# Optimization experiments

Measured on AMD Instinct MI355X. Metric: run time of the kernel, lower is better.

The kernel has to match this reference:

```python
import jax, jax.numpy as jnp
import numpy as np

B, T, I, H, O = 64, 512, 256, 512, 256

def setup_inputs() -> dict:
    key = jax.random.key(0)
    ks = jax.random.split(key, 12)
    s = 1.0 / np.sqrt(H)
    u = lambda k, shp: jax.random.uniform(k, shp, jnp.float32, -s, s)
    return {
        'x': jax.random.normal(ks[0], (B, T, I), jnp.float32),
        'w_ih0': u(ks[1], (H, I)),  'w_hh0': u(ks[2], (H, H)),
        'b_ih0': u(ks[3], (H,)),    'b_hh0': u(ks[4], (H,)),
        'w_ih1': u(ks[5], (H, H)),  'w_hh1': u(ks[6], (H, H)),
        'b_ih1': u(ks[7], (H,)),    'b_hh1': u(ks[8], (H,)),
        'fc_w': u(ks[9], (O, H)),   'fc_b': u(ks[10], (O,)),
    }

def _rnn_layer(inp, w_ih, w_hh, b_ih, b_hh):
    # inp: [B, T, F] -> precompute input projection once (one big GEMM)
    xp = jnp.einsum('btf,hf->bth', inp, w_ih) + b_ih + b_hh  # [B, T, H]
    def step(h, xt):
        h = jnp.tanh(xt + h @ w_hh.T)  # [B, H]
        return h, h
    h0 = jnp.zeros((inp.shape[0], w_hh.shape[0]), inp.dtype)
    hT, outs = jax.lax.scan(step, h0, jnp.swapaxes(xp, 0, 1))  # outs: [T, B, H]
    return jnp.swapaxes(outs, 0, 1), hT

def reference(x, w_ih0, w_hh0, b_ih0, b_hh0, w_ih1, w_hh1, b_ih1, b_hh1, fc_w, fc_b):
    out0, h0f = _rnn_layer(x, w_ih0, w_hh0, b_ih0, b_hh0)
    out1, h1f = _rnn_layer(out0, w_ih1, w_hh1, b_ih1, b_hh1)
    hidden = jnp.stack([h0f, h1f])                  # [n_layers, B, H]
    out = out1.reshape(-1, out1.shape[-1]) @ fc_w.T + fc_b  # [B*T, O]
    return out, hidden
```

## Files before the change

kernel.cpp:

```cpp
#include <hip/hip_runtime.h>

#define B_  64
#define T_  512
#define I_  256
#define H_  512
#define O_  256
#define JW  2
#define BS  16
#define NG  (B_ / BS)
#define SENT 0x7F7F7F7Fu
#define SLOT_BYTES 8192
#define BLK_SLOT_STRIDE 32768

typedef __attribute__((ext_vector_type(8))) __bf16 bf16x8;
typedef __attribute__((ext_vector_type(4))) float f32x4;
typedef unsigned int u32x4 __attribute__((ext_vector_type(4)));

__device__ __forceinline__ unsigned short f2bf(float f) {
    unsigned int u = __float_as_uint(f);
    unsigned int r = (u + 0x7fffu + ((u >> 16) & 1u)) >> 16;
    return (unsigned short)r;
}

__device__ __forceinline__ float tanh_fast(float x) {
    float e = __expf(2.0f * x);
    float d = e + 1.0f;
    float r;
    asm("v_rcp_f32 %0, %1" : "=v"(r) : "v"(d));
    return 1.0f - 2.0f * r;
}

__global__ void cvt_kernel(const float* __restrict__ in, unsigned short* __restrict__ out, int n4) {
    int i = blockIdx.x * blockDim.x + threadIdx.x;
    if (i >= n4) return;
    float4 f = reinterpret_cast<const float4*>(in)[i];
    ushort4 o;
    o.x = f2bf(f.x); o.y = f2bf(f.y); o.z = f2bf(f.z); o.w = f2bf(f.w);
    reinterpret_cast<ushort4*>(out)[i] = o;
}

__global__ __launch_bounds__(256) void gemm_kernel(
    const unsigned short* __restrict__ A,
    const unsigned short* __restrict__ Bw,
    const float* __restrict__ b0,
    const float* __restrict__ b1,
    float* __restrict__ C,
    int M, int N, int K)
{
    const int m0 = blockIdx.x * 64;
    const int n0 = blockIdx.y * 64;
    const int tid = threadIdx.x;
    const int wv = tid >> 6;
    const int l = tid & 63;
    const int lr = l & 15;
    const int lk = (l >> 4) * 8;
    const int arow = m0 + wv * 16 + lr;

    f32x4 acc[4] = {{0,0,0,0},{0,0,0,0},{0,0,0,0},{0,0,0,0}};
    const int nks = K / 32;
    for (int ks = 0; ks < nks; ++ks) {
        bf16x8 a = *reinterpret_cast<const bf16x8*>(A + (size_t)arow * K + ks * 32 + lk);
        #pragma unroll
        for (int nt = 0; nt < 4; ++nt) {
            bf16x8 b = *reinterpret_cast<const bf16x8*>(Bw + (size_t)(n0 + nt * 16 + lr) * K + ks * 32 + lk);
            acc[nt] = __builtin_amdgcn_mfma_f32_16x16x32_bf16(a, b, acc[nt], 0, 0, 0);
        }
    }
    #pragma unroll
    for (int nt = 0; nt < 4; ++nt) {
        #pragma unroll
        for (int r = 0; r < 4; ++r) {
            int row = m0 + wv * 16 + (l >> 4) * 4 + r;
            int col = n0 + nt * 16 + lr;
            float v = acc[nt][r];
            if (b0) v += b0[col];
            if (b1) v += b1[col];
            C[(size_t)row * N + col] = v;
        }
    }
}

#define LDW8(ARR, BASE) \
    asm volatile( \
        "global_load_dwordx4 %0, %8, %9 offset:0\n\t" \
        "global_load_dwordx4 %1, %8, %9 offset:64\n\t" \
        "global_load_dwordx4 %2, %8, %9 offset:128\n\t" \
        "global_load_dwordx4 %3, %8, %9 offset:192\n\t" \
        "global_load_dwordx4 %4, %8, %9 offset:256\n\t" \
        "global_load_dwordx4 %5, %8, %9 offset:320\n\t" \
        "global_load_dwordx4 %6, %8, %9 offset:384\n\t" \
        "global_load_dwordx4 %7, %8, %9 offset:448\n\t" \
        "s_waitcnt vmcnt(0)" \
        : "=&v"(ARR[0]), "=&v"(ARR[1]), "=&v"(ARR[2]), "=&v"(ARR[3]), \
          "=&v"(ARR[4]), "=&v"(ARR[5]), "=&v"(ARR[6]), "=&v"(ARR[7]) \
        : "v"(BASE), "s"(w))

#define STORE_SLOT_OUT(PK, VSLW, VOUT) \
    asm volatile( \
        "global_store_dword %16, %0, %21 sc0 sc1\n\t" \
        "global_store_dword %16, %1, %21 offset:512 sc0 sc1\n\t" \
        "global_store_dword %16, %2, %21 offset:1024 sc0 sc1\n\t" \
        "global_store_dword %16, %3, %21 offset:1536 sc0 sc1\n\t" \
        "global_store_dword %16, %4, %21 offset:32 sc0 sc1\n\t" \
        "global_store_dword %16, %5, %21 offset:544 sc0 sc1\n\t" \
        "global_store_dword %16, %6, %21 offset:1056 sc0 sc1\n\t" \
        "global_store_dword %16, %7, %21 offset:1568 sc0 sc1\n\t" \
        "global_store_dword %16, %8, %21 offset:64 sc0 sc1\n\t" \
        "global_store_dword %16, %9, %21 offset:576 sc0 sc1\n\t" \
        "global_store_dword %16, %10, %21 offset:1088 sc0 sc1\n\t" \
        "global_store_dword %16, %11, %21 offset:1600 sc0 sc1\n\t" \
        "global_store_dword %16, %12, %21 offset:96 sc0 sc1\n\t" \
        "global_store_dword %16, %13, %21 offset:608 sc0 sc1\n\t" \
        "global_store_dword %16, %14, %21 offset:1120 sc0 sc1\n\t" \
        "global_store_dword %16, %15, %21 offset:1632 sc0 sc1\n\t" \
        "global_store_dword %17, %0, %22\n\t" \
        "global_store_dword %18, %1, %22\n\t" \
        "global_store_dword %19, %2, %22\n\t" \
        "global_store_dword %20, %3, %22\n\t" \
        "global_store_dword %17, %4, %22 offset:32\n\t" \
        "global_store_dword %18, %5, %22 offset:32\n\t" \
        "global_store_dword %19, %6, %22 offset:32\n\t" \
        "global_store_dword %20, %7, %22 offset:32\n\t" \
        "global_store_dword %17, %8, %22 offset:64\n\t" \
        "global_store_dword %18, %9, %22 offset:64\n\t" \
        "global_store_dword %19, %10, %22 offset:64\n\t" \
        "global_store_dword %20, %11, %22 offset:64\n\t" \
        "global_store_dword %17, %12, %22 offset:96\n\t" \
        "global_store_dword %18, %13, %22 offset:96\n\t" \
        "global_store_dword %19, %14, %22 offset:96\n\t" \
        "global_store_dword %20, %15, %22 offset:96" \
        :: "v"(PK[0]), "v"(PK[1]), "v"(PK[2]), "v"(PK[3]), \
           "v"(PK[4]), "v"(PK[5]), "v"(PK[6]), "v"(PK[7]), \
           "v"(PK[8]), "v"(PK[9]), "v"(PK[10]), "v"(PK[11]), \
           "v"(PK[12]), "v"(PK[13]), "v"(PK[14]), "v"(PK[15]), \
           "v"(VSLW), "v"(VOUT[0]), "v"(VOUT[1]), "v"(VOUT[2]), "v"(VOUT[3]), \
           "s"(slots), "s"(out_bf) \
        : "memory")

__global__ __launch_bounds__(256, 1) void recur_kernel(
    const float* __restrict__ xp,
    const unsigned short* __restrict__ w,
    unsigned short* __restrict__ out_bf,
    float* __restrict__ h_final,
    unsigned short* __restrict__ slots)
{
    __shared__ __align__(16) unsigned short lds[16 * 280];

    const int bid = blockIdx.x;
    const int g   = bid >> 1;
    const int jw  = bid & 1;
    const int pjw = jw ^ 1;
    const int b0  = g * BS;
    const int tid = threadIdx.x;
    const int wv  = tid >> 6;
    const int l   = tid & 63;
    const int lr  = l & 15;
    const int lk  = (l >> 4) * 8;
    const int jn0 = jw * 256 + wv * 64;
    const int erow_l = (l >> 4) * 4;
    const int erow_g = b0 + erow_l;

    bf16x8 bwo[4][8], bwp[4][8];
    #pragma unroll
    for (int nt = 0; nt < 4; ++nt) {
        unsigned int vo = (unsigned)((jn0 + nt * 16 + lr) * (H_ * 2) + jw  * 512 + lk * 2);
        unsigned int vp = (unsigned)((jn0 + nt * 16 + lr) * (H_ * 2) + pjw * 512 + lk * 2);
        LDW8(bwo[nt], vo);
        LDW8(bwp[nt], vp);
    }

    unsigned int vxpr[4], vout[4];
    #pragma unroll
    for (int r = 0; r < 4; ++r) {
        vxpr[r] = (unsigned)((((erow_g + r) * T_) * H_ + jn0 + lr) * 4);
        vout[r] = (unsigned)(((erow_g + r) * T_) * H_ * 2 + (jn0 + lr) * 2);
    }
    const unsigned int slot_wr_b = (unsigned)(bid * BLK_SLOT_STRIDE);
    const unsigned int slot_rd_b = (unsigned)((bid ^ 1) * BLK_SLOT_STRIDE);
    const unsigned int vslr_base = slot_rd_b + (unsigned)(lr * 512 + lk * 2);
    const unsigned int vslw_base = slot_wr_b + (unsigned)(erow_l * 512 + (wv * 64 + lr) * 2);
    const unsigned int vsent_base = slot_rd_b + (unsigned)(wv * 2048 + l * 16);
    const u32x4 sentq = {SENT, SENT, SENT, SENT};

    {
        float xpr[16];
        asm volatile(
            "global_load_dword %0, %16, %20\n\t"
            "global_load_dword %1, %17, %20\n\t"
            "global_load_dword %2, %18, %20\n\t"
            "global_load_dword %3, %19, %20\n\t"
            "global_load_dword %4, %16, %20 offset:64\n\t"
            "global_load_dword %5, %17, %20 offset:64\n\t"
            "global_load_dword %6, %18, %20 offset:64\n\t"
            "global_load_dword %7, %19, %20 offset:64\n\t"
            "global_load_dword %8, %16, %20 offset:128\n\t"
            "global_load_dword %9, %17, %20 offset:128\n\t"
            "global_load_dword %10, %18, %20 offset:128\n\t"
            "global_load_dword %11, %19, %20 offset:128\n\t"
            "global_load_dword %12, %16, %20 offset:192\n\t"
            "global_load_dword %13, %17, %20 offset:192\n\t"
            "global_load_dword %14, %18, %20 offset:192\n\t"
            "global_load_dword %15, %19, %20 offset:192\n\t"
            "s_waitcnt vmcnt(0)"
            : "=&v"(xpr[0]), "=&v"(xpr[1]), "=&v"(xpr[2]), "=&v"(xpr[3]),
              "=&v"(xpr[4]), "=&v"(xpr[5]), "=&v"(xpr[6]), "=&v"(xpr[7]),
              "=&v"(xpr[8]), "=&v"(xpr[9]), "=&v"(xpr[10]), "=&v"(xpr[11]),
              "=&v"(xpr[12]), "=&v"(xpr[13]), "=&v"(xpr[14]), "=&v"(xpr[15])
            : "v"(vxpr[0]), "v"(vxpr[1]), "v"(vxpr[2]), "v"(vxpr[3]), "s"(xp));

        unsigned int pk[16];
        #pragma unroll
        for (int nt = 0; nt < 4; ++nt)
            #pragma unroll
            for (int r = 0; r < 4; ++r) {
                int i = nt * 4 + r;
                float hv = tanh_fast(xpr[i]);
                unsigned int mine = f2bf(hv);
                unsigned int oth = (unsigned int)__shfl_xor((int)mine, 1, 64);
                pk[i] = mine | (oth << 16);
            }
        if (!(lr & 1)) {
            unsigned int* lw = (unsigned int*)lds;
            const int cb = wv * 32 + (lr >> 1);
            #pragma unroll
            for (int nt = 0; nt < 4; ++nt)
                #pragma unroll
                for (int r = 0; r < 4; ++r)
                    lw[(erow_l + r) * 140 + cb + nt * 8] = pk[nt * 4 + r];
            unsigned int vslw = vslw_base + 1u * SLOT_BYTES;
            STORE_SLOT_OUT(pk, vslw, vout);
        }
        __syncthreads();
        #pragma unroll
        for (int r = 0; r < 4; ++r) { vxpr[r] += H_ * 4; vout[r] += H_ * 2; }
    }

    for (int t = 1; t < T_; ++t) {
        f32x4 acc[4] = {{0,0,0,0},{0,0,0,0},{0,0,0,0},{0,0,0,0}};
        {
            bf16x8 afo[8];
            const unsigned short* lrb = lds + lr * 280 + lk;
            #pragma unroll
            for (int i = 0; i < 8; ++i)
                afo[i] = *reinterpret_cast<const bf16x8*>(lrb + i * 32);
            #pragma unroll
            for (int i = 0; i < 8; ++i) {
                acc[0] = __builtin_amdgcn_mfma_f32_16x16x32_bf16(afo[i], bwo[0][i], acc[0], 0, 0, 0);
                acc[1] = __builtin_amdgcn_mfma_f32_16x16x32_bf16(afo[i], bwo[1][i], acc[1], 0, 0, 0);
                acc[2] = __builtin_amdgcn_mfma_f32_16x16x32_bf16(afo[i], bwo[2][i], acc[2], 0, 0, 0);
                acc[3] = __builtin_amdgcn_mfma_f32_16x16x32_bf16(afo[i], bwo[3][i], acc[3], 0, 0, 0);
            }
        }
        __builtin_amdgcn_sched_barrier(0);

        const unsigned int vslr = vslr_base + (unsigned)(t & 3) * SLOT_BYTES;
        float xpr[16];
        u32x4 afp[8];
        asm volatile(
            "global_load_dword %0, %24, %28\n\t"
            "global_load_dword %1, %25, %28\n\t"
            "global_load_dword %2, %26, %28\n\t"
            "global_load_dword %3, %27, %28\n\t"
            "global_load_dword %4, %24, %28 offset:64\n\t"
            "global_load_dword %5, %25, %28 offset:64\n\t"
            "global_load_dword %6, %26, %28 offset:64\n\t"
            "global_load_dword %7, %27, %28 offset:64\n\t"
            "global_load_dword %8, %24, %28 offset:128\n\t"
            "global_load_dword %9, %25, %28 offset:128\n\t"
            "global_load_dword %10, %26, %28 offset:128\n\t"
            "global_load_dword %11, %27, %28 offset:128\n\t"
            "global_load_dword %12, %24, %28 offset:192\n\t"
            "global_load_dword %13, %25, %28 offset:192\n\t"
            "global_load_dword %14, %26, %28 offset:192\n\t"
            "global_load_dword %15, %27, %28 offset:192\n\t"
            "global_load_dwordx4 %16, %29, %30 sc0 sc1\n\t"
            "global_load_dwordx4 %17, %29, %30 offset:64 sc0 sc1\n\t"
            "global_load_dwordx4 %18, %29, %30 offset:128 sc0 sc1\n\t"
            "global_load_dwordx4 %19, %29, %30 offset:192 sc0 sc1\n\t"
            "global_load_dwordx4 %20, %29, %30 offset:256 sc0 sc1\n\t"
            "global_load_dwordx4 %21, %29, %30 offset:320 sc0 sc1\n\t"
            "global_load_dwordx4 %22, %29, %30 offset:384 sc0 sc1\n\t"
            "global_load_dwordx4 %23, %29, %30 offset:448 sc0 sc1\n\t"
            "s_waitcnt vmcnt(0)"
            : "=&v"(xpr[0]), "=&v"(xpr[1]), "=&v"(xpr[2]), "=&v"(xpr[3]),
              "=&v"(xpr[4]), "=&v"(xpr[5]), "=&v"(xpr[6]), "=&v"(xpr[7]),
              "=&v"(xpr[8]), "=&v"(xpr[9]), "=&v"(xpr[10]), "=&v"(xpr[11]),
              "=&v"(xpr[12]), "=&v"(xpr[13]), "=&v"(xpr[14]), "=&v"(xpr[15]),
              "=&v"(afp[0]), "=&v"(afp[1]), "=&v"(afp[2]), "=&v"(afp[3]),
              "=&v"(afp[4]), "=&v"(afp[5]), "=&v"(afp[6]), "=&v"(afp[7])
            : "v"(vxpr[0]), "v"(vxpr[1]), "v"(vxpr[2]), "v"(vxpr[3]),
              "s"(xp), "v"(vslr), "s"(slots));

        int bad = 0;
        #pragma unroll
        for (int i = 0; i < 8; ++i)
            #pragma unroll
            for (int j = 0; j < 4; ++j)
                bad |= (afp[i][j] == SENT);
        while (__any(bad)) {
            asm volatile(
                "global_load_dwordx4 %0, %8, %9 sc0 sc1\n\t"
                "global_load_dwordx4 %1, %8, %9 offset:64 sc0 sc1\n\t"
                "global_load_dwordx4 %2, %8, %9 offset:128 sc0 sc1\n\t"
                "global_load_dwordx4 %3, %8, %9 offset:192 sc0 sc1\n\t"
                "global_load_dwordx4 %4, %8, %9 offset:256 sc0 sc1\n\t"
                "global_load_dwordx4 %5, %8, %9 offset:320 sc0 sc1\n\t"
                "global_load_dwordx4 %6, %8, %9 offset:384 sc0 sc1\n\t"
                "global_load_dwordx4 %7, %8, %9 offset:448 sc0 sc1\n\t"
                "s_waitcnt vmcnt(0)"
                : "=&v"(afp[0]), "=&v"(afp[1]), "=&v"(afp[2]), "=&v"(afp[3]),
                  "=&v"(afp[4]), "=&v"(afp[5]), "=&v"(afp[6]), "=&v"(afp[7])
                : "v"(vslr), "s"(slots));
            bad = 0;
            #pragma unroll
            for (int i = 0; i < 8; ++i)
                #pragma unroll
                for (int j = 0; j < 4; ++j)
                    bad |= (afp[i][j] == SENT);
        }
        __builtin_amdgcn_sched_barrier(0);

        #pragma unroll
        for (int i = 0; i < 8; ++i) {
            bf16x8 a = __builtin_bit_cast(bf16x8, afp[i]);
            acc[0] = __builtin_amdgcn_mfma_f32_16x16x32_bf16(a, bwp[0][i], acc[0], 0, 0, 0);
            acc[1] = __builtin_amdgcn_mfma_f32_16x16x32_bf16(a, bwp[1][i], acc[1], 0, 0, 0);
            acc[2] = __builtin_amdgcn_mfma_f32_16x16x32_bf16(a, bwp[2][i], acc[2], 0, 0, 0);
            acc[3] = __builtin_amdgcn_mfma_f32_16x16x32_bf16(a, bwp[3][i], acc[3], 0, 0, 0);
        }

        unsigned int pk[16];
        #pragma unroll
        for (int nt = 0; nt < 4; ++nt)
            #pragma unroll
            for (int r = 0; r < 4; ++r) {
                int i = nt * 4 + r;
                float pre = acc[nt][r] + xpr[i];
                float hv = tanh_fast(pre);
                if (t == T_ - 1)
                    h_final[(size_t)(erow_g + r) * H_ + jn0 + nt * 16 + lr] = hv;
                unsigned int mine = f2bf(hv);
                unsigned int oth = (unsigned int)__shfl_xor((int)mine, 1, 64);
                pk[i] = mine | (oth << 16);
            }
        if (!(lr & 1)) {
            unsigned int* lw = (unsigned int*)lds;
            const int cb = wv * 32 + (lr >> 1);
            #pragma unroll
            for (int nt = 0; nt < 4; ++nt)
                #pragma unroll
                for (int r = 0; r < 4; ++r)
                    lw[(erow_l + r) * 140 + cb + nt * 8] = pk[nt * 4 + r];
            unsigned int vslw = vslw_base + (unsigned)((t + 1) & 3) * SLOT_BYTES;
            STORE_SLOT_OUT(pk, vslw, vout);
        }

        __syncthreads();

        {
            unsigned int vs = vsent_base + (unsigned)(t & 3) * SLOT_BYTES;
            asm volatile(
                "global_store_dwordx4 %0, %1, %2 sc0 sc1\n\t"
                "global_store_dwordx4 %0, %1, %2 offset:1024 sc0 sc1"
                :: "v"(vs), "v"(sentq), "s"(slots) : "memory");
        }
        #pragma unroll
        for (int r = 0; r < 4; ++r) { vxpr[r] += H_ * 4; vout[r] += H_ * 2; }
    }
}

#define OFF_XBF    ((size_t)0)
#define OFF_WIH0   ((size_t)16777216)
#define OFF_WHH0   ((size_t)17039360)
#define OFF_WIH1   ((size_t)17563648)
#define OFF_WHH1   ((size_t)18087936)
#define OFF_FCW    ((size_t)18612224)
#define OFF_XP     ((size_t)18874368)
#define OFF_OUTBF  ((size_t)85983232)
#define OFF_SLOTS  ((size_t)119537664)
#define WS_NEED    ((size_t)119799808)

extern "C" void kernel_launch(void* const* d_in, const int* in_sizes, int n_in,
                              void* d_out, int out_size, void* d_ws, size_t ws_size,
                              hipStream_t stream) {
    if (ws_size < WS_NEED) return;
    const float* x     = (const float*)d_in[0];
    const float* w_ih0 = (const float*)d_in[1];
    const float* w_hh0 = (const float*)d_in[2];
    const float* b_ih0 = (const float*)d_in[3];
    const float* b_hh0 = (const float*)d_in[4];
    const float* w_ih1 = (const float*)d_in[5];
    const float* w_hh1 = (const float*)d_in[6];
    const float* b_ih1 = (const float*)d_in[7];
    const float* b_hh1 = (const float*)d_in[8];
    const float* fc_w  = (const float*)d_in[9];
    const float* fc_b  = (const float*)d_in[10];

    char* ws = (char*)d_ws;
    unsigned short* x_bf     = (unsigned short*)(ws + OFF_XBF);
    unsigned short* w_ih0_bf = (unsigned short*)(ws + OFF_WIH0);
    unsigned short* w_hh0_bf = (unsigned short*)(ws + OFF_WHH0);
    unsigned short* w_ih1_bf = (unsigned short*)(ws + OFF_WIH1);
    unsigned short* w_hh1_bf = (unsigned short*)(ws + OFF_WHH1);
    unsigned short* fc_w_bf  = (unsigned short*)(ws + OFF_FCW);
    float*          xp       = (float*)(ws + OFF_XP);
    unsigned short* out_bf   = (unsigned short*)(ws + OFF_OUTBF);
    unsigned short* slots    = (unsigned short*)(ws + OFF_SLOTS);

    float* out  = (float*)d_out;
    float* hid0 = out + (size_t)B_ * T_ * O_;
    float* hid1 = hid0 + (size_t)B_ * H_;

    hipMemsetAsync(ws + OFF_SLOTS, 0x7F, 262144, stream);

    auto cvt = [&](const float* in, unsigned short* o, int n) {
        int n4 = n / 4;
        cvt_kernel<<<(n4 + 255) / 256, 256, 0, stream>>>(in, o, n4);
    };
    cvt(x,     x_bf,     B_ * T_ * I_);
    cvt(w_ih0, w_ih0_bf, H_ * I_);
    cvt(w_hh0, w_hh0_bf, H_ * H_);
    cvt(w_ih1, w_ih1_bf, H_ * H_);
    cvt(w_hh1, w_hh1_bf, H_ * H_);
    cvt(fc_w,  fc_w_bf,  O_ * H_);

    const int M = B_ * T_;

    gemm_kernel<<<dim3(M / 64, H_ / 64), 256, 0, stream>>>(
        x_bf, w_ih0_bf, b_ih0, b_hh0, xp, M, H_, I_);

    recur_kernel<<<NG * JW, 256, 0, stream>>>(xp, w_hh0_bf, out_bf, hid0, slots);

    gemm_kernel<<<dim3(M / 64, H_ / 64), 256, 0, stream>>>(
        out_bf, w_ih1_bf, b_ih1, b_hh1, xp, M, H_, H_);

    hipMemsetAsync(ws + OFF_SLOTS, 0x7F, 262144, stream);

    recur_kernel<<<NG * JW, 256, 0, stream>>>(xp, w_hh1_bf, out_bf, hid1, slots);

    gemm_kernel<<<dim3(M / 64, O_ / 64), 256, 0, stream>>>(
        out_bf, fc_w_bf, fc_b, nullptr, out, M, O_, H_);
}
```

Measured before the change: 3.599 ms.

## Process two batch groups per block and permute xp layout for vector loads

The recurrence kernel now runs on 4 blocks instead of 8. Each block pair covers 32 batch rows split into two 16-row groups, so the MFMA work per exchanged step doubles and the number of cross-block handshakes per batch row halves. The input-projection GEMM writes its output in a permuted column order, which lets each lane fetch its 16 xp values with four dwordx4 loads instead of sixteen scalar loads. In exchange, each block does twice the serial work per timestep, and the two groups' peer loads and spin-waits are serialized within the step.

```diff
diff --git a/kernel.cpp b/kernel.cpp
--- a/kernel.cpp
+++ b/kernel.cpp
@@ -5,12 +5,9 @@
 #define I_  256
 #define H_  512
 #define O_  256
-#define JW  2
-#define BS  16
-#define NG  (B_ / BS)
 #define SENT 0x7F7F7F7Fu
-#define SLOT_BYTES 8192
-#define BLK_SLOT_STRIDE 32768
+#define SLOT_BYTES 16384
+#define BLK_SLOT_ELEMS 32768
 
 typedef __attribute__((ext_vector_type(8))) __bf16 bf16x8;
 typedef __attribute__((ext_vector_type(4))) float f32x4;
@@ -45,7 +42,7 @@
     const float* __restrict__ b0,
     const float* __restrict__ b1,
     float* __restrict__ C,
-    int M, int N, int K)
+    int M, int N, int K, int perm)
 {
     const int m0 = blockIdx.x * 64;
     const int n0 = blockIdx.y * 64;
@@ -75,7 +72,8 @@
             float v = acc[nt][r];
             if (b0) v += b0[col];
             if (b1) v += b1[col];
-            C[(size_t)row * N + col] = v;
+            int cs = perm ? ((col & 15) * 32 + (col >> 4)) : col;
+            C[(size_t)row * N + cs] = v;
         }
     }
 }
@@ -95,7 +93,51 @@
           "=&v"(ARR[4]), "=&v"(ARR[5]), "=&v"(ARR[6]), "=&v"(ARR[7]) \
         : "v"(BASE), "s"(w))
 
-#define STORE_SLOT_OUT(PK, VSLW, VOUT) \
+#define LOAD_XP_PEER(XPQ, AFP, VSLR, XPBASE, SLBASE) \
+    asm volatile( \
+        "global_load_dwordx4 %0, %12, %16\n\t" \
+        "global_load_dwordx4 %1, %13, %16\n\t" \
+        "global_load_dwordx4 %2, %14, %16\n\t" \
+        "global_load_dwordx4 %3, %15, %16\n\t" \
+        "global_load_dwordx4 %4, %17, %18 sc0 sc1\n\t" \
+        "global_load_dwordx4 %5, %17, %18 offset:64 sc0 sc1\n\t" \
+        "global_load_dwordx4 %6, %17, %18 offset:128 sc0 sc1\n\t" \
+        "global_load_dwordx4 %7, %17, %18 offset:192 sc0 sc1\n\t" \
+        "global_load_dwordx4 %8, %17, %18 offset:256 sc0 sc1\n\t" \
+        "global_load_dwordx4 %9, %17, %18 offset:320 sc0 sc1\n\t" \
+        "global_load_dwordx4 %10, %17, %18 offset:384 sc0 sc1\n\t" \
+        "global_load_dwordx4 %11, %17, %18 offset:448 sc0 sc1\n\t" \
+        "s_waitcnt vmcnt(0)" \
+        : "=&v"(XPQ[0]), "=&v"(XPQ[1]), "=&v"(XPQ[2]), "=&v"(XPQ[3]), \
+          "=&v"(AFP[0]), "=&v"(AFP[1]), "=&v"(AFP[2]), "=&v"(AFP[3]), \
+          "=&v"(AFP[4]), "=&v"(AFP[5]), "=&v"(AFP[6]), "=&v"(AFP[7]) \
+        : "v"(vxpr[0]), "v"(vxpr[1]), "v"(vxpr[2]), "v"(vxpr[3]), \
+          "s"(XPBASE), "v"(VSLR), "s"(SLBASE))
+
+#define RETRY8(AFP, VSLR, SLBASE) \
+    asm volatile( \
+        "global_load_dwordx4 %0, %8, %9 sc0 sc1\n\t" \
+        "global_load_dwordx4 %1, %8, %9 offset:64 sc0 sc1\n\t" \
+        "global_load_dwordx4 %2, %8, %9 offset:128 sc0 sc1\n\t" \
+        "global_load_dwordx4 %3, %8, %9 offset:192 sc0 sc1\n\t" \
+        "global_load_dwordx4 %4, %8, %9 offset:256 sc0 sc1\n\t" \
+        "global_load_dwordx4 %5, %8, %9 offset:320 sc0 sc1\n\t" \
+        "global_load_dwordx4 %6, %8, %9 offset:384 sc0 sc1\n\t" \
+        "global_load_dwordx4 %7, %8, %9 offset:448 sc0 sc1\n\t" \
+        "s_waitcnt vmcnt(0)" \
+        : "=&v"(AFP[0]), "=&v"(AFP[1]), "=&v"(AFP[2]), "=&v"(AFP[3]), \
+          "=&v"(AFP[4]), "=&v"(AFP[5]), "=&v"(AFP[6]), "=&v"(AFP[7]) \
+        : "v"(VSLR), "s"(SLBASE))
+
+#define SENT_CHECK(AFP, BAD) \
+    { BAD = 0; \
+      _Pragma("unroll") \
+      for (int _i = 0; _i < 8; ++_i) \
+          _Pragma("unroll") \
+          for (int _j = 0; _j < 4; ++_j) \
+              BAD |= (AFP[_i][_j] == SENT); }
+
+#define STORE_SLOT_OUT(PK, VSLW, SLWB, OUTB) \
     asm volatile( \
         "global_store_dword %16, %0, %21 sc0 sc1\n\t" \
         "global_store_dword %16, %1, %21 offset:512 sc0 sc1\n\t" \
@@ -133,8 +175,8 @@
            "v"(PK[4]), "v"(PK[5]), "v"(PK[6]), "v"(PK[7]), \
            "v"(PK[8]), "v"(PK[9]), "v"(PK[10]), "v"(PK[11]), \
            "v"(PK[12]), "v"(PK[13]), "v"(PK[14]), "v"(PK[15]), \
-           "v"(VSLW), "v"(VOUT[0]), "v"(VOUT[1]), "v"(VOUT[2]), "v"(VOUT[3]), \
-           "s"(slots), "s"(out_bf) \
+           "v"(VSLW), "v"(vout[0]), "v"(vout[1]), "v"(vout[2]), "v"(vout[3]), \
+           "s"(SLWB), "s"(OUTB) \
         : "memory")
 
 __global__ __launch_bounds__(256, 1) void recur_kernel(
@@ -144,13 +186,14 @@
     float* __restrict__ h_final,
     unsigned short* __restrict__ slots)
 {
-    __shared__ __align__(16) unsigned short lds[16 * 280];
+    __shared__ __align__(16) unsigned short lds[32 * 280];
 
     const int bid = blockIdx.x;
-    const int g   = bid >> 1;
+    const int g01 = bid >> 1;
     const int jw  = bid & 1;
     const int pjw = jw ^ 1;
-    const int b0  = g * BS;
+    const int b0A = g01 * 32;
+    const int b0B = g01 * 32 + 16;
     const int tid = threadIdx.x;
     const int wv  = tid >> 6;
     const int l   = tid & 63;
@@ -158,7 +201,16 @@
     const int lk  = (l >> 4) * 8;
     const int jn0 = jw * 256 + wv * 64;
     const int erow_l = (l >> 4) * 4;
-    const int erow_g = b0 + erow_l;
+
+    const float*          xpA  = xp     + (size_t)b0A * T_ * H_;
+    const float*          xpB  = xp     + (size_t)b0B * T_ * H_;
+    unsigned short*       outA = out_bf + (size_t)b0A * T_ * H_;
+    unsigned short*       outB = out_bf + (size_t)b0B * T_ * H_;
+    float*                hfA  = h_final + (size_t)b0A * H_;
+    float*                hfB  = h_final + (size_t)b0B * H_;
+    unsigned short*       slW  = slots + (size_t)bid * BLK_SLOT_ELEMS;
+    const unsigned short* slRA = slots + (size_t)(bid ^ 1) * BLK_SLOT_ELEMS;
+    const unsigned short* slRB = slRA + 4096;
 
     bf16x8 bwo[4][8], bwp[4][8];
     #pragma unroll
@@ -172,197 +224,158 @@
     unsigned int vxpr[4], vout[4];
     #pragma unroll
     for (int r = 0; r < 4; ++r) {
-        vxpr[r] = (unsigned)((((erow_g + r) * T_) * H_ + jn0 + lr) * 4);
-        vout[r] = (unsigned)(((erow_g + r) * T_) * H_ * 2 + (jn0 + lr) * 2);
-    }
-    const unsigned int slot_wr_b = (unsigned)(bid * BLK_SLOT_STRIDE);
-    const unsigned int slot_rd_b = (unsigned)((bid ^ 1) * BLK_SLOT_STRIDE);
-    const unsigned int vslr_base = slot_rd_b + (unsigned)(lr * 512 + lk * 2);
-    const unsigned int vslw_base = slot_wr_b + (unsigned)(erow_l * 512 + (wv * 64 + lr) * 2);
-    const unsigned int vsent_base = slot_rd_b + (unsigned)(wv * 2048 + l * 16);
+        vxpr[r] = (unsigned)(((erow_l + r) * T_ * H_ + lr * 32 + jw * 16 + wv * 4) * 4);
+        vout[r] = (unsigned)(((erow_l + r) * T_) * H_ * 2 + (jn0 + lr) * 2);
+    }
+    const unsigned int vslr0 = (unsigned)(lr * 512 + lk * 2);
+    const unsigned int vslw0 = (unsigned)(erow_l * 512 + (wv * 64 + lr) * 2);
+    const unsigned int vsent0 = (unsigned)(tid * 64);
     const u32x4 sentq = {SENT, SENT, SENT, SENT};
-
-    {
-        float xpr[16];
+    const int cb = wv * 32 + (lr >> 1);
+
+    #pragma unroll
+    for (int grp = 0; grp < 2; ++grp) {
+        const float* xpg = grp ? xpB : xpA;
+        unsigned short* outg = grp ? outB : outA;
+        f32x4 xpq[4];
         asm volatile(
-            "global_load_dword %0, %16, %20\n\t"
-            "global_load_dword %1, %17, %20\n\t"
-            "global_load_dword %2, %18, %20\n\t"
-            "global_load_dword %3, %19, %20\n\t"
-            "global_load_dword %4, %16, %20 offset:64\n\t"
-            "global_load_dword %5, %17, %20 offset:64\n\t"
-            "global_load_dword %6, %18, %20 offset:64\n\t"
-            "global_load_dword %7, %19, %20 offset:64\n\t"
-            "global_load_dword %8, %16, %20 offset:128\n\t"
-            "global_load_dword %9, %17, %20 offset:128\n\t"
-            "global_load_dword %10, %18, %20 offset:128\n\t"
-            "global_load_dword %11, %19, %20 offset:128\n\t"
-            "global_load_dword %12, %16, %20 offset:192\n\t"
-            "global_load_dword %13, %17, %20 offset:192\n\t"
-            "global_load_dword %14, %18, %20 offset:192\n\t"
-            "global_load_dword %15, %19, %20 offset:192\n\t"
+            "global_load_dwordx4 %0, %4, %8\n\t"
+            "global_load_dwordx4 %1, %5, %8\n\t"
+            "global_load_dwordx4 %2, %6, %8\n\t"
+            "global_load_dwordx4 %3, %7, %8\n\t"
             "s_waitcnt vmcnt(0)"
-            : "=&v"(xpr[0]), "=&v"(xpr[1]), "=&v"(xpr[2]), "=&v"(xpr[3]),
-              "=&v"(xpr[4]), "=&v"(xpr[5]), "=&v"(xpr[6]), "=&v"(xpr[7]),
-              "=&v"(xpr[8]), "=&v"(xpr[9]), "=&v"(xpr[10]), "=&v"(xpr[11]),
-              "=&v"(xpr[12]), "=&v"(xpr[13]), "=&v"(xpr[14]), "=&v"(xpr[15])
-            : "v"(vxpr[0]), "v"(vxpr[1]), "v"(vxpr[2]), "v"(vxpr[3]), "s"(xp));
-
+            : "=&v"(xpq[0]), "=&v"(xpq[1]), "=&v"(xpq[2]), "=&v"(xpq[3])
+            : "v"(vxpr[0]), "v"(vxpr[1]), "v"(vxpr[2]), "v"(vxpr[3]), "s"(xpg));
         unsigned int pk[16];
         #pragma unroll
         for (int nt = 0; nt < 4; ++nt)
             #pragma unroll
             for (int r = 0; r < 4; ++r) {
-                int i = nt * 4 + r;
-                float hv = tanh_fast(xpr[i]);
+                float hv = tanh_fast(xpq[r][nt]);
                 unsigned int mine = f2bf(hv);
                 unsigned int oth = (unsigned int)__shfl_xor((int)mine, 1, 64);
-                pk[i] = mine | (oth << 16);
+                pk[nt * 4 + r] = mine | (oth << 16);
             }
         if (!(lr & 1)) {
             unsigned int* lw = (unsigned int*)lds;
-            const int cb = wv * 32 + (lr >> 1);
             #pragma unroll
             for (int nt = 0; nt < 4; ++nt)
                 #pragma unroll
                 for (int r = 0; r < 4; ++r)
-                    lw[(erow_l + r) * 140 + cb + nt * 8] = pk[nt * 4 + r];
-            unsigned int vslw = vslw_base + 1u * SLOT_BYTES;
-            STORE_SLOT_OUT(pk, vslw, vout);
-        }
-        __syncthreads();
-        #pragma unroll
-        for (int r = 0; r < 4; ++r) { vxpr[r] += H_ * 4; vout[r] += H_ * 2; }
-    }
+                    lw[(grp * 16 + erow_l + r) * 140 + cb + nt * 8] = pk[nt * 4 + r];
+            unsigned int vslw = vslw0 + 1u * SLOT_BYTES + (unsigned)(grp * 8192);
+            STORE_SLOT_OUT(pk, vslw, slW, outg);
+        }
+    }
+    __syncthreads();
+    #pragma unroll
+    for (int r = 0; r < 4; ++r) { vxpr[r] += H_ * 4; vout[r] += H_ * 2; }
 
     for (int t = 1; t < T_; ++t) {
-        f32x4 acc[4] = {{0,0,0,0},{0,0,0,0},{0,0,0,0},{0,0,0,0}};
+        f32x4 accA[4] = {{0,0,0,0},{0,0,0,0},{0,0,0,0},{0,0,0,0}};
+        f32x4 accB[4] = {{0,0,0,0},{0,0,0,0},{0,0,0,0},{0,0,0,0}};
         {
             bf16x8 afo[8];
             const unsigned short* lrb = lds + lr * 280 + lk;
             #pragma unroll
-            for (int i = 0; i < 8; ++i)
-                afo[i] = *reinterpret_cast<const bf16x8*>(lrb + i * 32);
+            for (int i = 0; i < 8; ++i) afo[i] = *reinterpret_cast<const bf16x8*>(lrb + i * 32);
             #pragma unroll
             for (int i = 0; i < 8; ++i) {
-                acc[0] = __builtin_amdgcn_mfma_f32_16x16x32_bf16(afo[i], bwo[0][i], acc[0], 0, 0, 0);
-                acc[1] = __builtin_amdgcn_mfma_f32_16x16x32_bf16(afo[i], bwo[1][i], acc[1], 0, 0, 0);
-                acc[2] = __builtin_amdgcn_mfma_f32_16x16x32_bf16(afo[i], bwo[2][i], acc[2], 0, 0, 0);
-                acc[3] = __builtin_amdgcn_mfma_f32_16x16x32_bf16(afo[i], bwo[3][i], acc[3], 0, 0, 0);
+                accA[0] = __builtin_amdgcn_mfma_f32_16x16x32_bf16(afo[i], bwo[0][i], accA[0], 0, 0, 0);
+                accA[1] = __builtin_amdgcn_mfma_f32_16x16x32_bf16(afo[i], bwo[1][i], accA[1], 0, 0, 0);
+                accA[2] = __builtin_amdgcn_mfma_f32_16x16x32_bf16(afo[i], bwo[2][i], accA[2], 0, 0, 0);
+                accA[3] = __builtin_amdgcn_mfma_f32_16x16x32_bf16(afo[i], bwo[3][i], accA[3], 0, 0, 0);
             }
         }
+        {
+            bf16x8 afo[8];
+            const unsigned short* lrb = lds + (16 + lr) * 280 + lk;
+            #pragma unroll
+            for (int i = 0; i < 8; ++i) afo[i] = *reinterpret_cast<const bf16x8*>(lrb + i * 32);
+            #pragma unroll
+            for (int i = 0; i < 8; ++i) {
+                accB[0] = __builtin_amdgcn_mfma_f32_16x16x32_bf16(afo[i], bwo[0][i], accB[0], 0, 0, 0);
+                accB[1] = __builtin_amdgcn_mfma_f32_16x16x32_bf16(afo[i], bwo[1][i], accB[1], 0, 0, 0);
+                accB[2] = __builtin_amdgcn_mfma_f32_16x16x32_bf16(afo[i], bwo[2][i], accB[2], 0, 0, 0);
+                accB[3] = __builtin_amdgcn_mfma_f32_16x16x32_bf16(afo[i], bwo[3][i], accB[3], 0, 0, 0);
+            }
+        }
         __builtin_amdgcn_sched_barrier(0);
 
-        const unsigned int vslr = vslr_base + (unsigned)(t & 3) * SLOT_BYTES;
-        float xpr[16];
-        u32x4 afp[8];
-        asm volatile(
-            "global_load_dword %0, %24, %28\n\t"
-            "global_load_dword %1, %25, %28\n\t"
-            "global_load_dword %2, %26, %28\n\t"
-            "global_load_dword %3, %27, %28\n\t"
-            "global_load_dword %4, %24, %28 offset:64\n\t"
-            "global_load_dword %5, %25, %28 offset:64\n\t"
-            "global_load_dword %6, %26, %28 offset:64\n\t"
-            "global_load_dword %7, %27, %28 offset:64\n\t"
-            "global_load_dword %8, %24, %28 offset:128\n\t"
-            "global_load_dword %9, %25, %28 offset:128\n\t"
-            "global_load_dword %10, %26, %28 offset:128\n\t"
-            "global_load_dword %11, %27, %28 offset:128\n\t"
-            "global_load_dword %12, %24, %28 offset:192\n\t"
-            "global_load_dword %13, %25, %28 offset:192\n\t"
-            "global_load_dword %14, %26, %28 offset:192\n\t"
-            "global_load_dword %15, %27, %28 offset:192\n\t"
-            "global_load_dwordx4 %16, %29, %30 sc0 sc1\n\t"
-            "global_load_dwordx4 %17, %29, %30 offset:64 sc0 sc1\n\t"
-            "global_load_dwordx4 %18, %29, %30 offset:128 sc0 sc1\n\t"
-            "global_load_dwordx4 %19, %29, %30 offset:192 sc0 sc1\n\t"
-            "global_load_dwordx4 %20, %29, %30 offset:256 sc0 sc1\n\t"
-            "global_load_dwordx4 %21, %29, %30 offset:320 sc0 sc1\n\t"
-            "global_load_dwordx4 %22, %29, %30 offset:384 sc0 sc1\n\t"
-            "global_load_dwordx4 %23, %29, %30 offset:448 sc0 sc1\n\t"
-            "s_waitcnt vmcnt(0)"
-            : "=&v"(xpr[0]), "=&v"(xpr[1]), "=&v"(xpr[2]), "=&v"(xpr[3]),
-              "=&v"(xpr[4]), "=&v"(xpr[5]), "=&v"(xpr[6]), "=&v"(xpr[7]),
-              "=&v"(xpr[8]), "=&v"(xpr[9]), "=&v"(xpr[10]), "=&v"(xpr[11]),
-              "=&v"(xpr[12]), "=&v"(xpr[13]), "=&v"(xpr[14]), "=&v"(xpr[15]),
-              "=&v"(afp[0]), "=&v"(afp[1]), "=&v"(afp[2]), "=&v"(afp[3]),
-              "=&v"(afp[4]), "=&v"(afp[5]), "=&v"(afp[6]), "=&v"(afp[7])
-            : "v"(vxpr[0]), "v"(vxpr[1]), "v"(vxpr[2]), "v"(vxpr[3]),
-              "s"(xp), "v"(vslr), "s"(slots));
-
-        int bad = 0;
-        #pragma unroll
-        for (int i = 0; i < 8; ++i)
-            #pragma unroll
-            for (int j = 0; j < 4; ++j)
-                bad |= (afp[i][j] == SENT);
-        while (__any(bad)) {
-            asm volatile(
-                "global_load_dwordx4 %0, %8, %9 sc0 sc1\n\t"
-                "global_load_dwordx4 %1, %8, %9 offset:64 sc0 sc1\n\t"
-                "global_load_dwordx4 %2, %8, %9 offset:128 sc0 sc1\n\t"
-                "global_load_dwordx4 %3, %8, %9 offset:192 sc0 sc1\n\t"
-                "global_load_dwordx4 %4, %8, %9 offset:256 sc0 sc1\n\t"
-                "global_load_dwordx4 %5, %8, %9 offset:320 sc0 sc1\n\t"
-                "global_load_dwordx4 %6, %8, %9 offset:384 sc0 sc1\n\t"
-                "global_load_dwordx4 %7, %8, %9 offset:448 sc0 sc1\n\t"
-                "s_waitcnt vmcnt(0)"
-                : "=&v"(afp[0]), "=&v"(afp[1]), "=&v"(afp[2]), "=&v"(afp[3]),
-                  "=&v"(afp[4]), "=&v"(afp[5]), "=&v"(afp[6]), "=&v"(afp[7])
-                : "v"(vslr), "s"(slots));
-            bad = 0;
-            #pragma unroll
-            for (int i = 0; i < 8; ++i)
-                #pragma unroll
-                for (int j = 0; j < 4; ++j)
-                    bad |= (afp[i][j] == SENT);
-        }
+        const unsigned int vslr = vslr0 + (unsigned)(t & 3) * SLOT_BYTES;
+
+        f32x4 xpqA[4];
+        u32x4 afpA[8];
+        LOAD_XP_PEER(xpqA, afpA, vslr, xpA, slRA);
+        int bad;
+        SENT_CHECK(afpA, bad);
+        while (__any(bad)) { RETRY8(afpA, vslr, slRA); SENT_CHECK(afpA, bad); }
         __builtin_amdgcn_sched_barrier(0);
-
         #pragma unroll
         for (int i = 0; i < 8; ++i) {
-            bf16x8 a = __builtin_bit_cast(bf16x8, afp[i]);
-            acc[0] = __builtin_amdgcn_mfma_f32_16x16x32_bf16(a, bwp[0][i], acc[0], 0, 0, 0);
-            acc[1] = __builtin_amdgcn_mfma_f32_16x16x32_bf16(a, bwp[1][i], acc[1], 0, 0, 0);
-            acc[2] = __builtin_amdgcn_mfma_f32_16x16x32_bf16(a, bwp[2][i], acc[2], 0, 0, 0);
-            acc[3] = __builtin_amdgcn_mfma_f32_16x16x32_bf16(a, bwp[3][i], acc[3], 0, 0, 0);
-        }
-
-        unsigned int pk[16];
-        #pragma unroll
-        for (int nt = 0; nt < 4; ++nt)
-            #pragma unroll
-            for (int r = 0; r < 4; ++r) {
-                int i = nt * 4 + r;
-                float pre = acc[nt][r] + xpr[i];
-                float hv = tanh_fast(pre);
-                if (t == T_ - 1)
-                    h_final[(size_t)(erow_g + r) * H_ + jn0 + nt * 16 + lr] = hv;
-                unsigned int mine = f2bf(hv);
-                unsigned int oth = (unsigned int)__shfl_xor((int)mine, 1, 64);
-                pk[i] = mine | (oth << 16);
-            }
-        if (!(lr & 1)) {
-            unsigned int* lw = (unsigned int*)lds;
-            const int cb = wv * 32 + (lr >> 1);
+            bf16x8 a = __builtin_bit_cast(bf16x8, afpA[i]);
+            accA[0] = __builtin_amdgcn_mfma_f32_16x16x32_bf16(a, bwp[0][i], accA[0], 0, 0, 0);
+            accA[1] = __builtin_amdgcn_mfma_f32_16x16x32_bf16(a, bwp[1][i], accA[1], 0, 0, 0);
+            accA[2] = __builtin_amdgcn_mfma_f32_16x16x32_bf16(a, bwp[2][i], accA[2], 0, 0, 0);
+            accA[3] = __builtin_amdgcn_mfma_f32_16x16x32_bf16(a, bwp[3][i], accA[3], 0, 0, 0);
+        }
+
+        f32x4 xpqB[4];
+        u32x4 afpB[8];
+        LOAD_XP_PEER(xpqB, afpB, vslr, xpB, slRB);
+        SENT_CHECK(afpB, bad);
+        while (__any(bad)) { RETRY8(afpB, vslr, slRB); SENT_CHECK(afpB, bad); }
+        __builtin_amdgcn_sched_barrier(0);
+        #pragma unroll
+        for (int i = 0; i < 8; ++i) {
+            bf16x8 a = __builtin_bit_cast(bf16x8, afpB[i]);
+            accB[0] = __builtin_amdgcn_mfma_f32_16x16x32_bf16(a, bwp[0][i], accB[0], 0, 0, 0);
+            accB[1] = __builtin_amdgcn_mfma_f32_16x16x32_bf16(a, bwp[1][i], accB[1], 0, 0, 0);
+            accB[2] = __builtin_amdgcn_mfma_f32_16x16x32_bf16(a, bwp[2][i], accB[2], 0, 0, 0);
+            accB[3] = __builtin_amdgcn_mfma_f32_16x16x32_bf16(a, bwp[3][i], accB[3], 0, 0, 0);
+        }
+
+        #pragma unroll
+        for (int grp = 0; grp < 2; ++grp) {
+            f32x4* acc = grp ? accB : accA;
+            f32x4* xpq = grp ? xpqB : xpqA;
+            float* hfg = grp ? hfB : hfA;
+            unsigned short* outg = grp ? outB : outA;
+            unsigned int pk[16];
             #pragma unroll
             for (int nt = 0; nt < 4; ++nt)
                 #pragma unroll
-                for (int r = 0; r < 4; ++r)
-                    lw[(erow_l + r) * 140 + cb + nt * 8] = pk[nt * 4 + r];
-            unsigned int vslw = vslw_base + (unsigned)((t + 1) & 3) * SLOT_BYTES;
-            STORE_SLOT_OUT(pk, vslw, vout);
+                for (int r = 0; r < 4; ++r) {
+                    float pre = acc[nt][r] + xpq[r][nt];
+                    float hv = tanh_fast(pre);
+                    if (t == T_ - 1)
+                        hfg[(size_t)(erow_l + r) * H_ + jn0 + nt * 16 + lr] = hv;
+                    unsigned int mine = f2bf(hv);
+                    unsigned int oth = (unsigned int)__shfl_xor((int)mine, 1, 64);
+                    pk[nt * 4 + r] = mine | (oth << 16);
+                }
+            if (!(lr & 1)) {
+                unsigned int* lw = (unsigned int*)lds;
+                #pragma unroll
+                for (int nt = 0; nt < 4; ++nt)
+                    #pragma unroll
+                    for (int r = 0; r < 4; ++r)
+                        lw[(grp * 16 + erow_l + r) * 140 + cb + nt * 8] = pk[nt * 4 + r];
+                unsigned int vslw = vslw0 + (unsigned)((t + 1) & 3) * SLOT_BYTES + (unsigned)(grp * 8192);
+                STORE_SLOT_OUT(pk, vslw, slW, outg);
+            }
         }
 
         __syncthreads();
 
         {
-            unsigned int vs = vsent_base + (unsigned)(t & 3) * SLOT_BYTES;
+            unsigned int vs = vsent0 + (unsigned)(t & 3) * SLOT_BYTES;
             asm volatile(
                 "global_store_dwordx4 %0, %1, %2 sc0 sc1\n\t"
-                "global_store_dwordx4 %0, %1, %2 offset:1024 sc0 sc1"
-                :: "v"(vs), "v"(sentq), "s"(slots) : "memory");
+                "global_store_dwordx4 %0, %1, %2 offset:16 sc0 sc1\n\t"
+                "global_store_dwordx4 %0, %1, %2 offset:32 sc0 sc1\n\t"
+                "global_store_dwordx4 %0, %1, %2 offset:48 sc0 sc1"
+                :: "v"(vs), "v"(sentq), "s"(slRA) : "memory");
         }
         #pragma unroll
         for (int r = 0; r < 4; ++r) { vxpr[r] += H_ * 4; vout[r] += H_ * 2; }
@@ -427,17 +440,17 @@
     const int M = B_ * T_;
 
     gemm_kernel<<<dim3(M / 64, H_ / 64), 256, 0, stream>>>(
-        x_bf, w_ih0_bf, b_ih0, b_hh0, xp, M, H_, I_);
-
-    recur_kernel<<<NG * JW, 256, 0, stream>>>(xp, w_hh0_bf, out_bf, hid0, slots);
+        x_bf, w_ih0_bf, b_ih0, b_hh0, xp, M, H_, I_, 1);
+
+    recur_kernel<<<4, 256, 0, stream>>>(xp, w_hh0_bf, out_bf, hid0, slots);
 
     gemm_kernel<<<dim3(M / 64, H_ / 64), 256, 0, stream>>>(
-        out_bf, w_ih1_bf, b_ih1, b_hh1, xp, M, H_, H_);
+        out_bf, w_ih1_bf, b_ih1, b_hh1, xp, M, H_, H_, 1);
 
     hipMemsetAsync(ws + OFF_SLOTS, 0x7F, 262144, stream);
 
-    recur_kernel<<<NG * JW, 256, 0, stream>>>(xp, w_hh1_bf, out_bf, hid1, slots);
+    recur_kernel<<<4, 256, 0, stream>>>(xp, w_hh1_bf, out_bf, hid1, slots);
 
     gemm_kernel<<<dim3(M / 64, O_ / 64), 256, 0, stream>>>(
-        out_bf, fc_w_bf, fc_b, nullptr, out, M, O_, H_);
-}
+        out_bf, fc_w_bf, fc_b, nullptr, out, M, O_, H_, 0);
+}
```

Measured after the change: 6.931 ms. 92.6% more time.
